# Optimization experiments

Measured on AMD Instinct MI355X. Metric: run time of the kernel, lower is better.

The kernel has to match this reference:

```python
import jax, jax.numpy as jnp
import numpy as np

B, CQ, CVK, L, H = 4, 256, 256, 2048, 8
D = CVK // H  # depth per head = 32
EPS = 1e-5    # BatchNorm eps


def setup_inputs() -> dict:
    key = jax.random.key(0)
    ks = jax.random.split(key, 32)
    n = lambda i, s, sc=1.0: jax.random.normal(ks[i], s, dtype=jnp.float32) * sc
    u = lambda i, s: jax.random.uniform(ks[i], s, dtype=jnp.float32, minval=0.5, maxval=1.5)
    inp = {
        'v': n(0, (B, CVK, L)), 'k': n(1, (B, CVK, L)), 'q': n(2, (B, CQ, L)),
        # trainable positional encodings (pe_q: image_shape_q, pe_vk: image_shape_vk)
        'pe_q': n(3, (CQ, L)), 'pe_vk': n(4, (CVK, L)),
        # W_query / W_key / W_value: Conv1d(kernel=1) weight [out,in] + bias, then BatchNorm1d (eval mode)
        'wq': n(5, (CVK, CQ), 0.05), 'bq': n(6, (CVK,), 0.05),
        'gq': 1.0 + n(7, (CVK,), 0.1), 'betaq': n(8, (CVK,), 0.1), 'mq': n(9, (CVK,), 0.1), 'varq': u(10, (CVK,)),
        'wk': n(11, (CVK, CVK), 0.05), 'bk': n(12, (CVK,), 0.05),
        'gk': 1.0 + n(13, (CVK,), 0.1), 'betak': n(14, (CVK,), 0.1), 'mk': n(15, (CVK,), 0.1), 'vark': u(16, (CVK,)),
        'wv': n(17, (CVK, CVK), 0.05), 'bv': n(18, (CVK,), 0.05),
        'gv': 1.0 + n(19, (CVK,), 0.1), 'betav': n(20, (CVK,), 0.1), 'mv': n(21, (CVK,), 0.1), 'varv': u(22, (CVK,)),
        # out_proj (zero-init in original; randomized here so gradients are non-trivial)
        'wo': n(23, (CQ, CVK), 0.05), 'bo': n(24, (CQ,), 0.05),
    }
    return inp


def _conv1(x, w, b):  # 1x1 conv == channel matmul: [b,c,l] -> [b,o,l]
    return jnp.einsum('oc,bcl->bol', w, x) + b[None, :, None]


def _bn(x, g, beta, mean, var):  # eval-mode BatchNorm1d over channel dim
    scale = g / jnp.sqrt(var + EPS)
    return (x - mean[:, None]) * scale[:, None] + beta[:, None]


def _mha(v, k, q, pe_q, pe_vk, wq, bq, gq, betaq, mq, varq,
         wk, bk, gk, betak, mk, vark, wv, bv, gv, betav, mv, varv, wo, bo):
    q_orig = q
    b = q.shape[0]
    vv = v + pe_vk[None]
    kk = k + pe_vk[None]
    qq = q + pe_q[None]
    qp = _bn(_conv1(qq, wq, bq), gq, betaq, mq, varq)   # [b, CVK, L]
    kp = _bn(_conv1(kk, wk, bk), gk, betak, mk, vark)
    vp = _bn(_conv1(vv, wv, bv), gv, betav, mv, varv)
    # split heads: [b, H, D, L]
    qh = qp.reshape(b, H, D, -1)
    kh = kp.reshape(b, H, D, -1)
    vh = vp.reshape(b, H, D, -1)
    # scaled dot-product attention over sequence dim (l: query pos, m: key pos)
    scores = jnp.einsum('bhdl,bhdm->bhlm', qh, kh) / jnp.sqrt(jnp.float32(D))
    p = jax.nn.softmax(scores, axis=-1)
    a = jnp.einsum('bhlm,bhdm->bhdl', p, vh)            # [b, H, D, L]
    a = a.reshape(b, H * D, -1)                          # [b, CVK, L]
    out = _conv1(a, wo, bo)                              # [b, CQ, L]
    return q_orig + out


def reference(v, k, q, pe_q, pe_vk, wq, bq, gq, betaq, mq, varq,
              wk, bk, gk, betak, mk, vark, wv, bv, gv, betav, mv, varv, wo, bo):
    return _mha(v, k, q, pe_q, pe_vk, wq, bq, gq, betaq, mq, varq,
                wk, bk, gk, betak, mk, vark, wv, bv, gv, betav, mv, varv, wo, bo)
```

## Files before the change

### kernel.cpp

```cpp
#include <hip/hip_runtime.h>
#include <hip/hip_bf16.h>

#define BB 4
#define CC 256
#define LL 2048
#define HH 8
#define DD 32
#define EPSV 1e-5f

typedef __bf16 bf16x8 __attribute__((ext_vector_type(8)));
typedef __bf16 bf16x4 __attribute__((ext_vector_type(4)));
typedef __bf16 bf16x2 __attribute__((ext_vector_type(2)));
typedef float  f32x4  __attribute__((ext_vector_type(4)));
typedef float  f32x16 __attribute__((ext_vector_type(16)));
typedef unsigned int u32x4 __attribute__((ext_vector_type(4)));

static __device__ __forceinline__ unsigned pkbf(float lo, float hi) {
    bf16x2 p; p[0] = (__bf16)lo; p[1] = (__bf16)hi;
    return __builtin_bit_cast(unsigned, p);
}

__global__ __launch_bounds__(512) void qkv_gemm_kernel(
    const float* __restrict__ qin, const float* __restrict__ kin,
    const float* __restrict__ vin,
    const float* __restrict__ peq, const float* __restrict__ pevk,
    const float* __restrict__ wq, const float* __restrict__ bq,
    const float* __restrict__ gq, const float* __restrict__ betaq,
    const float* __restrict__ mq, const float* __restrict__ varq,
    const float* __restrict__ wk, const float* __restrict__ bk,
    const float* __restrict__ gk, const float* __restrict__ betak,
    const float* __restrict__ mk, const float* __restrict__ vark,
    const float* __restrict__ wv, const float* __restrict__ bv,
    const float* __restrict__ gv, const float* __restrict__ betav,
    const float* __restrict__ mv, const float* __restrict__ varv,
    __bf16* __restrict__ qTo, __bf16* __restrict__ kTo, __bf16* __restrict__ vNo,
    float qscale)
{
    __shared__ __align__(16) __bf16 Wl[64][136];
    __shared__ __align__(16) __bf16 Xl[128][136];
    __bf16 (*Tl)[72] = (__bf16(*)[72])Xl;

    const int z = blockIdx.z;
    const int which = z >> 2;
    const int b = z & 3;
    const float* X    = which==0 ? qin : (which==1 ? kin : vin);
    const float* pe   = which==0 ? peq : pevk;
    const float* W    = which==0 ? wq  : (which==1 ? wk  : wv);
    const float* bia  = which==0 ? bq  : (which==1 ? bk  : bv);
    const float* gam  = which==0 ? gq  : (which==1 ? gk  : gv);
    const float* bet  = which==0 ? betaq : (which==1 ? betak : betav);
    const float* mea  = which==0 ? mq  : (which==1 ? mk  : mv);
    const float* var  = which==0 ? varq : (which==1 ? vark : varv);
    const float extra = (which==0) ? qscale : 1.0f;

    const int lt = blockIdx.x * 128;
    const int ot = blockIdx.y * 64;
    const int t  = threadIdx.x;
    const int wvi = t >> 6;
    const int wm = wvi >> 2;
    const int wn = wvi & 3;
    const int l  = t & 63;
    const int lq = l & 15;
    const int g  = l >> 4;

    f32x4 acc[2][2];
    #pragma unroll
    for (int mi = 0; mi < 2; ++mi)
        #pragma unroll
        for (int ni = 0; ni < 2; ++ni) acc[mi][ni] = (f32x4){0.f,0.f,0.f,0.f};

    for (int ks = 0; ks < 2; ++ks) {
        __syncthreads();
        #pragma unroll
        for (int i = 0; i < 4; ++i) {
            const int idx = i * 512 + t;
            const int row = idx >> 5;
            const int ch  = idx & 31;
            const int o   = ot + row;
            const float sc = gam[o] * rsqrtf(var[o] + EPSV) * extra;
            const float4 w4 = *(const float4*)&W[(size_t)o * CC + ks * 128 + ch * 4];
            bf16x4 wb;
            wb[0] = (__bf16)(w4.x * sc); wb[1] = (__bf16)(w4.y * sc);
            wb[2] = (__bf16)(w4.z * sc); wb[3] = (__bf16)(w4.w * sc);
            *(bf16x4*)&Wl[row][ch * 4] = wb;
        }
        #pragma unroll
        for (int i = 0; i < 2; ++i) {
            const int slot = i * 512 + t;
            const int lp = slot & 63;
            const int co = slot >> 6;
            const float* xp = &X[(size_t)(b * CC + ks * 128 + co * 8) * LL + lt + lp * 2];
            const float* pp = &pe[(size_t)(ks * 128 + co * 8) * LL + lt + lp * 2];
            bf16x8 lo, hi;
            #pragma unroll
            for (int j = 0; j < 8; ++j) {
                const float2 a = *(const float2*)&xp[(size_t)j * LL];
                const float2 p = *(const float2*)&pp[(size_t)j * LL];
                lo[j] = (__bf16)(a.x + p.x);
                hi[j] = (__bf16)(a.y + p.y);
            }
            *(bf16x8*)&Xl[lp * 2    ][co * 8] = lo;
            *(bf16x8*)&Xl[lp * 2 + 1][co * 8] = hi;
        }
        __syncthreads();

        #pragma unroll
        for (int kk = 0; kk < 4; ++kk) {
            bf16x8 af[2], bfr[2];
            #pragma unroll
            for (int mi = 0; mi < 2; ++mi)
                af[mi] = *(const bf16x8*)&Wl[wm * 32 + mi * 16 + lq][kk * 32 + g * 8];
            #pragma unroll
            for (int ni = 0; ni < 2; ++ni)
                bfr[ni] = *(const bf16x8*)&Xl[wn * 32 + ni * 16 + lq][kk * 32 + g * 8];
            #pragma unroll
            for (int mi = 0; mi < 2; ++mi)
                #pragma unroll
                for (int ni = 0; ni < 2; ++ni)
                    acc[mi][ni] = __builtin_amdgcn_mfma_f32_16x16x32_bf16(
                        af[mi], bfr[ni], acc[mi][ni], 0, 0, 0);
        }
    }

    float bb[2][4];
    #pragma unroll
    for (int mi = 0; mi < 2; ++mi) {
        const int o4 = ot + wm * 32 + mi * 16 + g * 4;
        const float4 b4 = *(const float4*)&bia[o4];
        const float4 g4 = *(const float4*)&gam[o4];
        const float4 v4 = *(const float4*)&var[o4];
        const float4 m4 = *(const float4*)&mea[o4];
        const float4 t4 = *(const float4*)&bet[o4];
        const float bs[4] = {b4.x,b4.y,b4.z,b4.w};
        const float gs[4] = {g4.x,g4.y,g4.z,g4.w};
        const float vs[4] = {v4.x,v4.y,v4.z,v4.w};
        const float ms[4] = {m4.x,m4.y,m4.z,m4.w};
        const float ts[4] = {t4.x,t4.y,t4.z,t4.w};
        #pragma unroll
        for (int r = 0; r < 4; ++r) {
            const float sc = gs[r] * rsqrtf(vs[r] + EPSV);
            bb[mi][r] = ((bs[r] - ms[r]) * sc + ts[r]) * extra;
        }
    }

    if (which < 2) {
        __bf16* outT = which==0 ? qTo : kTo;
        __syncthreads();
        #pragma unroll
        for (int mi = 0; mi < 2; ++mi) {
            #pragma unroll
            for (int ni = 0; ni < 2; ++ni) {
                bf16x4 pv;
                #pragma unroll
                for (int r = 0; r < 4; ++r) pv[r] = (__bf16)(acc[mi][ni][r] + bb[mi][r]);
                *(bf16x4*)&Tl[wn * 32 + ni * 16 + lq][wm * 32 + mi * 16 + g * 4] = pv;
            }
        }
        __syncthreads();
        #pragma unroll
        for (int i = 0; i < 2; ++i) {
            const int idx = i * 512 + t;
            const int lrow = idx >> 3, ch = idx & 7;
            *(bf16x8*)&outT[(size_t)(b * LL + lt + lrow) * CC + ot + ch * 8] =
                *(const bf16x8*)&Tl[lrow][ch * 8];
        }
    } else {
        #pragma unroll
        for (int mi = 0; mi < 2; ++mi) {
            #pragma unroll
            for (int ni = 0; ni < 2; ++ni) {
                const int col = lt + wn * 32 + ni * 16 + lq;
                #pragma unroll
                for (int r = 0; r < 4; ++r) {
                    const int o = ot + wm * 32 + mi * 16 + g * 4 + r;
                    vNo[(size_t)(b * CC + o) * LL + col] = (__bf16)(acc[mi][ni][r] + bb[mi][r]);
                }
            }
        }
    }
}

__global__ __launch_bounds__(256) void attn_mfma_kernel(
    const __bf16* __restrict__ qT, const __bf16* __restrict__ kT,
    const __bf16* __restrict__ vN, __bf16* __restrict__ aT)
{
    __shared__ __align__(16) __bf16 KB[2][128 * 32];
    __shared__ __align__(16) __bf16 VB[2][32 * 128];

    const int qb = blockIdx.x;
    const int h  = blockIdx.y;
    const int b  = blockIdx.z;
    const int t  = threadIdx.x;
    const int w  = t >> 6;
    const int l  = t & 63;
    const int lq = l & 31;
    const int hi = l >> 5;

    const int q0 = qb * 128 + w * 32;

    const __bf16* qrow = qT + ((size_t)(b * LL) + q0 + lq) * CC + h * DD;
    const bf16x8 qf0 = *(const bf16x8*)&qrow[hi * 8];
    const bf16x8 qf1 = *(const bf16x8*)&qrow[16 + hi * 8];

    const __bf16* kTb = kT + (size_t)(b * LL) * CC + h * DD;
    const __bf16* vNb = vN + ((size_t)(b * CC) + h * DD) * LL;

    const int s0 = t, s1 = 256 + t;
    const int sk0 = s0 >> 2, sp0 = s0 & 3;
    const int sk1 = s1 >> 2, sp1 = s1 & 3;
    const int sd0 = s0 >> 4, sv0 = s0 & 15;
    const int sd1 = s1 >> 4, sv1 = s1 & 15;
    const int kw0 = sk0 * 32 + (sp0 ^ ((sk0 >> 1) & 3)) * 8;
    const int kw1 = sk1 * 32 + (sp1 ^ ((sk1 >> 1) & 3)) * 8;
    const int vw0 = sd0 * 128 + (sv0 ^ (sd0 & 7)) * 8;
    const int vw1 = sd1 * 128 + (sv1 ^ (sd1 & 7)) * 8;

    bf16x8 kr0, kr1, vr0, vr1;
    #define LOADREGS(KT0) \
        kr0 = *(const bf16x8*)&kTb[(size_t)((KT0) + sk0) * CC + sp0 * 8]; \
        kr1 = *(const bf16x8*)&kTb[(size_t)((KT0) + sk1) * CC + sp1 * 8]; \
        vr0 = *(const bf16x8*)&vNb[(size_t)sd0 * LL + (KT0) + sv0 * 8];   \
        vr1 = *(const bf16x8*)&vNb[(size_t)sd1 * LL + (KT0) + sv1 * 8];
    #define WRITEBUF(BUF) \
        *(bf16x8*)&KB[BUF][kw0] = kr0; *(bf16x8*)&KB[BUF][kw1] = kr1; \
        *(bf16x8*)&VB[BUF][vw0] = vr0; *(bf16x8*)&VB[BUF][vw1] = vr1;

    LOADREGS(0)
    WRITEBUF(0)
    LOADREGS(128)

    f32x16 O;
    #pragma unroll
    for (int r = 0; r < 16; ++r) O[r] = 0.f;
    float ssum = 0.f;

    const int NT = LL / 128;
    for (int it = 0; it < NT; ++it) {
        const int buf = it & 1;
        __syncthreads();
        const __bf16* KBb = KB[buf];
        const __bf16* VBb = VB[buf];

        #pragma unroll
        for (int kb = 0; kb < 128; kb += 32) {
            const int key = kb + lq;
            const int ksw = (key >> 1) & 3;
            f32x16 S;
            #pragma unroll
            for (int r = 0; r < 16; ++r) S[r] = 0.f;
            {
                const bf16x8 kf0 = *(const bf16x8*)&KBb[key * 32 + ((hi    ) ^ ksw) * 8];
                const bf16x8 kf1 = *(const bf16x8*)&KBb[key * 32 + ((2 + hi) ^ ksw) * 8];
                __builtin_amdgcn_s_setprio(1);
                S = __builtin_amdgcn_mfma_f32_32x32x16_bf16(kf0, qf0, S, 0, 0, 0);
                S = __builtin_amdgcn_mfma_f32_32x32x16_bf16(kf1, qf1, S, 0, 0, 0);
                __builtin_amdgcn_s_setprio(0);
            }
            float e[16];
            #pragma unroll
            for (int r = 0; r < 16; ++r) e[r] = __builtin_amdgcn_exp2f(S[r]);
            float s = 0.f;
            #pragma unroll
            for (int r = 0; r < 16; r += 4) s += (e[r] + e[r+1]) + (e[r+2] + e[r+3]);
            ssum += s;
            unsigned a[8];
            #pragma unroll
            for (int i = 0; i < 8; ++i) a[i] = pkbf(e[2*i], e[2*i+1]);
            #pragma unroll
            for (int c = 0; c < 2; ++c) {
                unsigned w0 = a[4*c+0], w1 = a[4*c+1], w2 = a[4*c+2], w3 = a[4*c+3];
                asm volatile("v_permlane32_swap_b32 %0, %1" : "+v"(w0), "+v"(w2));
                asm volatile("v_permlane32_swap_b32 %0, %1" : "+v"(w1), "+v"(w3));
                u32x4 pv4 = {w0, w1, w2, w3};
                const bf16x8 pf = __builtin_bit_cast(bf16x8, pv4);
                const int slot = (kb >> 3) + 2 * c + hi;
                const bf16x8 vf = *(const bf16x8*)&VBb[lq * 128 + (slot ^ (lq & 7)) * 8];
                __builtin_amdgcn_s_setprio(1);
                O = __builtin_amdgcn_mfma_f32_32x32x16_bf16(vf, pf, O, 0, 0, 0);
                __builtin_amdgcn_s_setprio(0);
            }
        }

        if (it + 1 < NT) { WRITEBUF(buf ^ 1) }
        if (it + 2 < NT) { LOADREGS((it + 2) * 128) }
    }
    #undef LOADREGS
    #undef WRITEBUF

    ssum += __shfl_xor(ssum, 32);
    const float inv = 1.f / ssum;

    __bf16* arow = aT + ((size_t)(b * LL) + q0 + lq) * CC + h * DD;
    #pragma unroll
    for (int gi = 0; gi < 4; ++gi) {
        bf16x4 ov;
        #pragma unroll
        for (int r = 0; r < 4; ++r) ov[r] = (__bf16)(O[4*gi + r] * inv);
        *(bf16x4*)&arow[8 * gi + 4 * hi] = ov;
    }
}

__global__ __launch_bounds__(256) void outproj_kernel(
    const float* __restrict__ W, const __bf16* __restrict__ X,
    const float* __restrict__ bias, const float* __restrict__ resid,
    float* __restrict__ outF)
{
    __shared__ __align__(16) __bf16 Wl[64][136];
    __shared__ __align__(16) __bf16 Xl[64][136];

    const int lt = blockIdx.x * 64;
    const int ot = blockIdx.y * 64;
    const int b  = blockIdx.z;
    const int t  = threadIdx.x;
    const int wvi = t >> 6;
    const int wm = wvi >> 1;
    const int wn = wvi & 1;
    const int l  = t & 63;
    const int lq = l & 15;
    const int g  = l >> 4;

    f32x4 acc[2][2];
    #pragma unroll
    for (int mi = 0; mi < 2; ++mi)
        #pragma unroll
        for (int ni = 0; ni < 2; ++ni) acc[mi][ni] = (f32x4){0.f,0.f,0.f,0.f};

    for (int ks = 0; ks < 2; ++ks) {
        __syncthreads();
        #pragma unroll
        for (int i = 0; i < 8; ++i) {
            const int idx = i * 256 + t;
            const int row = idx >> 5;
            const int ch  = idx & 31;
            const float4 w4 = *(const float4*)&W[(size_t)(ot + row) * CC + ks * 128 + ch * 4];
            bf16x4 wb;
            wb[0] = (__bf16)w4.x; wb[1] = (__bf16)w4.y;
            wb[2] = (__bf16)w4.z; wb[3] = (__bf16)w4.w;
            *(bf16x4*)&Wl[row][ch * 4] = wb;
        }
        #pragma unroll
        for (int i = 0; i < 4; ++i) {
            const int idx = i * 256 + t;
            const int row = idx >> 4, ch = idx & 15;
            *(bf16x8*)&Xl[row][ch * 8] =
                *(const bf16x8*)&X[(size_t)(b * LL + lt + row) * CC + ks * 128 + ch * 8];
        }
        __syncthreads();

        #pragma unroll
        for (int kk = 0; kk < 4; ++kk) {
            bf16x8 af[2], bfr[2];
            #pragma unroll
            for (int mi = 0; mi < 2; ++mi)
                af[mi] = *(const bf16x8*)&Wl[wm * 32 + mi * 16 + lq][kk * 32 + g * 8];
            #pragma unroll
            for (int ni = 0; ni < 2; ++ni)
                bfr[ni] = *(const bf16x8*)&Xl[wn * 32 + ni * 16 + lq][kk * 32 + g * 8];
            #pragma unroll
            for (int mi = 0; mi < 2; ++mi)
                #pragma unroll
                for (int ni = 0; ni < 2; ++ni)
                    acc[mi][ni] = __builtin_amdgcn_mfma_f32_16x16x32_bf16(
                        af[mi], bfr[ni], acc[mi][ni], 0, 0, 0);
        }
    }

    #pragma unroll
    for (int mi = 0; mi < 2; ++mi) {
        const float4 b4 = *(const float4*)&bias[ot + wm * 32 + mi * 16 + g * 4];
        const float bb[4] = {b4.x, b4.y, b4.z, b4.w};
        #pragma unroll
        for (int ni = 0; ni < 2; ++ni) {
            const int col = lt + wn * 32 + ni * 16 + lq;
            #pragma unroll
            for (int r = 0; r < 4; ++r) {
                const int o = ot + wm * 32 + mi * 16 + g * 4 + r;
                const size_t a = (size_t)(b * CC + o) * LL + col;
                outF[a] = acc[mi][ni][r] + bb[r] + resid[a];
            }
        }
    }
}

extern "C" void kernel_launch(void* const* d_in, const int* in_sizes, int n_in,
                              void* d_out, int out_size, void* d_ws, size_t ws_size,
                              hipStream_t stream)
{
    const float* v     = (const float*)d_in[0];
    const float* k     = (const float*)d_in[1];
    const float* q     = (const float*)d_in[2];
    const float* pe_q  = (const float*)d_in[3];
    const float* pe_vk = (const float*)d_in[4];
    const float* wq    = (const float*)d_in[5];
    const float* bq    = (const float*)d_in[6];
    const float* gq    = (const float*)d_in[7];
    const float* betaq = (const float*)d_in[8];
    const float* mq    = (const float*)d_in[9];
    const float* varq  = (const float*)d_in[10];
    const float* wk    = (const float*)d_in[11];
    const float* bk    = (const float*)d_in[12];
    const float* gk    = (const float*)d_in[13];
    const float* betak = (const float*)d_in[14];
    const float* mk    = (const float*)d_in[15];
    const float* vark  = (const float*)d_in[16];
    const float* wv    = (const float*)d_in[17];
    const float* bv    = (const float*)d_in[18];
    const float* gv    = (const float*)d_in[19];
    const float* betav = (const float*)d_in[20];
    const float* mv    = (const float*)d_in[21];
    const float* varv  = (const float*)d_in[22];
    const float* wo    = (const float*)d_in[23];
    const float* bo    = (const float*)d_in[24];

    float* out = (float*)d_out;

    const size_t E = (size_t)BB * CC * LL;
    __bf16* qT  = (__bf16*)d_ws;
    __bf16* kT  = qT + E;
    __bf16* vN  = kT + E;
    __bf16* aT  = vN + E;

    const float qscale = 0.17677669529663687f * 1.4426950408889634f;

    hipLaunchKernelGGL(qkv_gemm_kernel, dim3(16, 4, 12), dim3(512), 0, stream,
                       q, k, v, pe_q, pe_vk,
                       wq, bq, gq, betaq, mq, varq,
                       wk, bk, gk, betak, mk, vark,
                       wv, bv, gv, betav, mv, varv,
                       qT, kT, vN, qscale);

    hipLaunchKernelGGL(attn_mfma_kernel, dim3(16, HH, BB), dim3(256), 0, stream,
                       qT, kT, vN, aT);

    hipLaunchKernelGGL(outproj_kernel, dim3(32, 4, 4), dim3(256), 0, stream,
                       wo, aT, bo, q, out);
}
```

Measured before the change: 65.11 us.

## Split attention keys across two wave halves and remap blocks per XCD

```diff
diff --git a/kernel.cpp b/kernel.cpp
--- a/kernel.cpp
+++ b/kernel.cpp
@@ -180,23 +180,31 @@
     }
 }
 
-__global__ __launch_bounds__(256) void attn_mfma_kernel(
+__global__ __launch_bounds__(512) void attn_mfma_kernel(
     const __bf16* __restrict__ qT, const __bf16* __restrict__ kT,
     const __bf16* __restrict__ vN, __bf16* __restrict__ aT)
 {
-    __shared__ __align__(16) __bf16 KB[2][128 * 32];
-    __shared__ __align__(16) __bf16 VB[2][32 * 128];
-
-    const int qb = blockIdx.x;
-    const int h  = blockIdx.y;
-    const int b  = blockIdx.z;
+    __shared__ __align__(16) __bf16 KB[2][2][4096];
+    __shared__ __align__(16) __bf16 VB[2][2][4096];
+
+    const int flat = blockIdx.x + 16 * (blockIdx.y + 8 * blockIdx.z);
+    const int xcd  = flat & 7;
+    const int ixc  = flat >> 3;
+    const int gidx = xcd + 8 * (ixc >> 4);
+    const int qb   = ixc & 15;
+    const int h    = gidx & 7;
+    const int b    = gidx >> 3;
+
     const int t  = threadIdx.x;
     const int w  = t >> 6;
+    const int hs = w >> 2;
+    const int wl = w & 3;
     const int l  = t & 63;
     const int lq = l & 31;
     const int hi = l >> 5;
 
-    const int q0 = qb * 128 + w * 32;
+    const int q0 = qb * 128 + wl * 32;
+    const int kbase = hs * 1024;
 
     const __bf16* qrow = qT + ((size_t)(b * LL) + q0 + lq) * CC + h * DD;
     const bf16x8 qf0 = *(const bf16x8*)&qrow[hi * 8];
@@ -205,7 +213,8 @@
     const __bf16* kTb = kT + (size_t)(b * LL) * CC + h * DD;
     const __bf16* vNb = vN + ((size_t)(b * CC) + h * DD) * LL;
 
-    const int s0 = t, s1 = 256 + t;
+    const int th = t & 255;
+    const int s0 = th, s1 = 256 + th;
     const int sk0 = s0 >> 2, sp0 = s0 & 3;
     const int sk1 = s1 >> 2, sp1 = s1 & 3;
     const int sd0 = s0 >> 4, sv0 = s0 & 15;
@@ -215,6 +224,9 @@
     const int vw0 = sd0 * 128 + (sv0 ^ (sd0 & 7)) * 8;
     const int vw1 = sd1 * 128 + (sv1 ^ (sd1 & 7)) * 8;
 
+    __bf16* KBw = &KB[hs][0][0];
+    __bf16* VBw = &VB[hs][0][0];
+
     bf16x8 kr0, kr1, vr0, vr1;
     #define LOADREGS(KT0) \
         kr0 = *(const bf16x8*)&kTb[(size_t)((KT0) + sk0) * CC + sp0 * 8]; \
@@ -222,24 +234,33 @@
         vr0 = *(const bf16x8*)&vNb[(size_t)sd0 * LL + (KT0) + sv0 * 8];   \
         vr1 = *(const bf16x8*)&vNb[(size_t)sd1 * LL + (KT0) + sv1 * 8];
     #define WRITEBUF(BUF) \
-        *(bf16x8*)&KB[BUF][kw0] = kr0; *(bf16x8*)&KB[BUF][kw1] = kr1; \
-        *(bf16x8*)&VB[BUF][vw0] = vr0; *(bf16x8*)&VB[BUF][vw1] = vr1;
-
-    LOADREGS(0)
+        *(bf16x8*)&KBw[(BUF) * 4096 + kw0] = kr0; \
+        *(bf16x8*)&KBw[(BUF) * 4096 + kw1] = kr1; \
+        *(bf16x8*)&VBw[(BUF) * 4096 + vw0] = vr0; \
+        *(bf16x8*)&VBw[(BUF) * 4096 + vw1] = vr1;
+
+    #define BARRIER() \
+        asm volatile("s_waitcnt lgkmcnt(0)\n\ts_barrier" ::: "memory"); \
+        __builtin_amdgcn_sched_barrier(0);
+
+    LOADREGS(kbase)
     WRITEBUF(0)
-    LOADREGS(128)
+    LOADREGS(kbase + 128)
 
     f32x16 O;
     #pragma unroll
     for (int r = 0; r < 16; ++r) O[r] = 0.f;
     float ssum = 0.f;
 
-    const int NT = LL / 128;
+    const int NT = 1024 / 128;
     for (int it = 0; it < NT; ++it) {
         const int buf = it & 1;
-        __syncthreads();
-        const __bf16* KBb = KB[buf];
-        const __bf16* VBb = VB[buf];
+        BARRIER()
+        if (it + 1 < NT) { WRITEBUF(buf ^ 1) }
+        if (it + 2 < NT) { LOADREGS(kbase + (it + 2) * 128) }
+
+        const __bf16* KBb = &KBw[buf * 4096];
+        const __bf16* VBb = &VBw[buf * 4096];
 
         #pragma unroll
         for (int kb = 0; kb < 128; kb += 32) {
@@ -251,10 +272,8 @@
             {
                 const bf16x8 kf0 = *(const bf16x8*)&KBb[key * 32 + ((hi    ) ^ ksw) * 8];
                 const bf16x8 kf1 = *(const bf16x8*)&KBb[key * 32 + ((2 + hi) ^ ksw) * 8];
-                __builtin_amdgcn_s_setprio(1);
                 S = __builtin_amdgcn_mfma_f32_32x32x16_bf16(kf0, qf0, S, 0, 0, 0);
                 S = __builtin_amdgcn_mfma_f32_32x32x16_bf16(kf1, qf1, S, 0, 0, 0);
-                __builtin_amdgcn_s_setprio(0);
             }
             float e[16];
             #pragma unroll
@@ -275,28 +294,41 @@
                 const bf16x8 pf = __builtin_bit_cast(bf16x8, pv4);
                 const int slot = (kb >> 3) + 2 * c + hi;
                 const bf16x8 vf = *(const bf16x8*)&VBb[lq * 128 + (slot ^ (lq & 7)) * 8];
-                __builtin_amdgcn_s_setprio(1);
                 O = __builtin_amdgcn_mfma_f32_32x32x16_bf16(vf, pf, O, 0, 0, 0);
-                __builtin_amdgcn_s_setprio(0);
-            }
-        }
-
-        if (it + 1 < NT) { WRITEBUF(buf ^ 1) }
-        if (it + 2 < NT) { LOADREGS((it + 2) * 128) }
+            }
+        }
     }
     #undef LOADREGS
     #undef WRITEBUF
+    #undef BARRIER
 
     ssum += __shfl_xor(ssum, 32);
-    const float inv = 1.f / ssum;
-
-    __bf16* arow = aT + ((size_t)(b * LL) + q0 + lq) * CC + h * DD;
-    #pragma unroll
-    for (int gi = 0; gi < 4; ++gi) {
-        bf16x4 ov;
-        #pragma unroll
-        for (int r = 0; r < 4; ++r) ov[r] = (__bf16)(O[4*gi + r] * inv);
-        *(bf16x4*)&arow[8 * gi + 4 * hi] = ov;
+
+    __syncthreads();
+    float* Of = (float*)&KB[0][0][0];
+    float* Sf = (float*)&VB[0][0][0];
+
+    const int qloc = wl * 32 + lq;
+    if (hs == 1) {
+        #pragma unroll
+        for (int gi = 0; gi < 4; ++gi)
+            #pragma unroll
+            for (int r = 0; r < 4; ++r)
+                Of[qloc * 33 + 8 * gi + 4 * hi + r] = O[4 * gi + r];
+        if (l < 32) Sf[qloc] = ssum;
+    }
+    __syncthreads();
+    if (hs == 0) {
+        const float inv = 1.f / (ssum + Sf[qloc]);
+        __bf16* arow = aT + ((size_t)(b * LL) + q0 + lq) * CC + h * DD;
+        #pragma unroll
+        for (int gi = 0; gi < 4; ++gi) {
+            bf16x4 ov;
+            #pragma unroll
+            for (int r = 0; r < 4; ++r)
+                ov[r] = (__bf16)((O[4*gi + r] + Of[qloc * 33 + 8 * gi + 4 * hi + r]) * inv);
+            *(bf16x4*)&arow[8 * gi + 4 * hi] = ov;
+        }
     }
 }
 
@@ -429,7 +461,7 @@
                        wv, bv, gv, betav, mv, varv,
                        qT, kT, vN, qscale);
 
-    hipLaunchKernelGGL(attn_mfma_kernel, dim3(16, HH, BB), dim3(256), 0, stream,
+    hipLaunchKernelGGL(attn_mfma_kernel, dim3(16, HH, BB), dim3(512), 0, stream,
                        qT, kT, vN, aT);
 
     hipLaunchKernelGGL(outproj_kernel, dim3(32, 4, 4), dim3(256), 0, stream,
```

After: 62.69 us. 3.7% less time.
